# Optimization experiments

Measured on AMD Instinct MI355X. Metric: run time of the kernel, lower is better.

The kernel has to match this reference:

```python
import jax, jax.numpy as jnp
import numpy as np

NUM_HEADS = 16


def setup_inputs() -> dict:
    key = jax.random.key(0)
    ks = jax.random.split(key, 9)
    B, N, E = 2, 2048, 1024
    s = 1.0 / np.sqrt(E).astype(np.float32)
    inp = {"x": jax.random.normal(ks[0], (B, N, E), jnp.float32)}
    names = ["q", "k", "v", "o"]
    for i, n in enumerate(names):
        inp[f"W{n}"] = jax.random.normal(ks[1 + 2 * i], (E, E), jnp.float32) * s
        inp[f"b{n}"] = jax.random.normal(ks[2 + 2 * i], (E,), jnp.float32) * 0.01
    return inp


def _feature(x):
    # act_fun = '1+elu'
    return jax.nn.elu(x) + 1.0


def reference(x, Wq, bq, Wk, bk, Wv, bv, Wo, bo):
    B, N, E = x.shape
    H = NUM_HEADS
    d = E // H

    def proj(t, W, b):  # torch nn.Linear: t @ W^T + b
        return t @ W.T + b

    def split_heads(t):  # (B,N,E) -> (B,H,N,d)
        return t.reshape(B, N, H, d).transpose(0, 2, 1, 3)

    q = _feature(split_heads(proj(x, Wq, bq)))
    k = _feature(split_heads(proj(x, Wk, bk)))
    v = split_heads(proj(x, Wv, bv))

    # causal linear attention: o_t = q_t @ cumsum_{s<=t} (k_s v_s^T)
    kv = jnp.cumsum(k[..., :, None] * v[..., None, :], axis=2)  # (B,H,N,d,d)
    o = jnp.einsum('bhnd,bhnde->bhne', q, kv)                   # (B,H,N,d)

    o = o.transpose(0, 2, 1, 3).reshape(B, N, E)
    return o @ Wo.T + bo
```

## Files before the change

kernel.cpp:

```cpp
#include <hip/hip_runtime.h>
#include <hip/hip_bf16.h>
#include <cmath>

typedef unsigned short u16;
typedef __bf16 bf16x8 __attribute__((ext_vector_type(8)));
typedef float  f32x4  __attribute__((ext_vector_type(4)));
typedef float  f4     __attribute__((ext_vector_type(4)));
typedef u16    us4    __attribute__((ext_vector_type(4)));

#define DEVFN __device__ __forceinline__

static constexpr int Bq = 2, Nq = 2048, Eq = 1024;
static constexpr int Mq = Bq * Nq;
static constexpr int CHK = 64;
static constexpr int NC  = Nq / CHK;
static constexpr int BH  = Bq * 16;

DEVFN u16 f2b(float f) {
    union { float f; unsigned int u; } x; x.f = f;
    unsigned int r = x.u + 0x7fffu + ((x.u >> 16) & 1u);
    return (u16)(r >> 16);
}
DEVFN float b2f(u16 v) {
    union { unsigned int u; float f; } x; x.u = ((unsigned int)v) << 16; return x.f;
}

DEVFN void gl_lds16(const u16* g, u16* l) {
    __builtin_amdgcn_global_load_lds(
        (const __attribute__((address_space(1))) unsigned int*)(g),
        (__attribute__((address_space(3))) unsigned int*)(l),
        16, 0, 0);
}

__global__ __launch_bounds__(256)
void cvt_all_kernel(const float* __restrict__ x,
                    const float* __restrict__ w0, const float* __restrict__ w1,
                    const float* __restrict__ w2, const float* __restrict__ w3,
                    u16* __restrict__ Xb, u16* __restrict__ Wb)
{
    const int blk = blockIdx.x;
    const float* s; u16* d; int i;
    if (blk < 4096) {
        i = blk * 256 + threadIdx.x;  s = x;  d = Xb;
    } else {
        const int wsel = (blk - 4096) >> 10;
        i = ((blk - 4096) & 1023) * 256 + threadIdx.x;
        s = (wsel == 0) ? w0 : (wsel == 1) ? w1 : (wsel == 2) ? w2 : w3;
        d = Wb + (size_t)wsel * (Eq * Eq);
    }
    f4 v = *reinterpret_cast<const f4*>(&s[(size_t)i * 4]);
    us4 p; p[0] = f2b(v[0]); p[1] = f2b(v[1]); p[2] = f2b(v[2]); p[3] = f2b(v[3]);
    *reinterpret_cast<us4*>(&d[(size_t)i * 4]) = p;
}

__global__ __launch_bounds__(512, 4)
void qkv_ring(const u16* __restrict__ X, const u16* __restrict__ W,
              const float* __restrict__ b0, const float* __restrict__ b1,
              const float* __restrict__ b2,
              u16* __restrict__ Qb, u16* __restrict__ Kb, u16* __restrict__ KbT,
              u16* __restrict__ VbT)
{
    constexpr int BUFU = 16384;
    __shared__ u16 lds[2 * BUFU];
    const int tid = threadIdx.x, wid = tid >> 6, lane = tid & 63;
    const int wr = (wid >> 1) * 32, wc = (wid & 1) * 64;
    const int fr = lane & 15, fq = lane >> 4;

    const int bid = blockIdx.x;
    const int fid = (bid & 7) * 96 + (bid >> 3);
    const int bx = fid % 24, by = fid / 24;
    const int m0 = by * 128, n0 = bx * 128;

    const int row0 = tid >> 3;
    const int sc   = ((tid & 7) ^ (row0 & 7)) * 8;
    const u16* gA = X + (size_t)(m0 + row0) * 1024 + sc;
    const u16* gB = W + (size_t)(n0 + row0) * 1024 + sc;
    const int dw = wid * 512;

    int aoff[2][2], boff[2][4];
#pragma unroll
    for (int kk = 0; kk < 2; ++kk) {
        const int slot = ((kk * 4 + fq) ^ (fr & 7)) << 3;
#pragma unroll
        for (int mi = 0; mi < 2; ++mi)
            aoff[kk][mi] = (wr + mi * 16 + fr) * 64 + slot;
#pragma unroll
        for (int ni = 0; ni < 4; ++ni)
            boff[kk][ni] = 8192 + (wc + ni * 16 + fr) * 64 + slot;
    }

#define STAGE(kt, bs) do { u16* _b = lds + (bs) * BUFU;                        \
        gl_lds16(gA + (kt) * 64,              _b + dw);                        \
        gl_lds16(gA + (kt) * 64 + 64 * 1024,  _b + 4096 + dw);                 \
        gl_lds16(gB + (kt) * 64,              _b + 8192 + dw);                 \
        gl_lds16(gB + (kt) * 64 + 64 * 1024,  _b + 12288 + dw); } while (0)

    STAGE(0, 0);
    asm volatile("s_waitcnt vmcnt(0)" ::: "memory");
    __builtin_amdgcn_sched_barrier(0);
    __builtin_amdgcn_s_barrier();

    f32x4 acc[2][4] = {};

    for (int t = 0; t < 16; ++t) {
        if (t + 1 < 16) STAGE(t + 1, (t + 1) & 1);
        const u16* buf = lds + (t & 1) * BUFU;
#pragma unroll
        for (int kk = 0; kk < 2; ++kk) {
            bf16x8 af[2], bfv[4];
#pragma unroll
            for (int mi = 0; mi < 2; ++mi)
                af[mi] = *reinterpret_cast<const bf16x8*>(&buf[aoff[kk][mi]]);
#pragma unroll
            for (int ni = 0; ni < 4; ++ni)
                bfv[ni] = *reinterpret_cast<const bf16x8*>(&buf[boff[kk][ni]]);
            __builtin_amdgcn_s_setprio(1);
#pragma unroll
            for (int mi = 0; mi < 2; ++mi)
#pragma unroll
                for (int ni = 0; ni < 4; ++ni)
                    acc[mi][ni] = __builtin_amdgcn_mfma_f32_16x16x32_bf16(
                        af[mi], bfv[ni], acc[mi][ni], 0, 0, 0);
            __builtin_amdgcn_s_setprio(0);
        }
        asm volatile("s_waitcnt vmcnt(0)" ::: "memory");
        __builtin_amdgcn_sched_barrier(0);
        __builtin_amdgcn_s_barrier();
    }
#undef STAGE

    const int nw  = n0 + wc;
    const int seg = nw >> 10;
    const float* bp = (seg == 0) ? b0 : (seg == 1) ? b1 : b2;
#pragma unroll
    for (int mi = 0; mi < 2; ++mi)
#pragma unroll
        for (int ni = 0; ni < 4; ++ni) {
            const int nl    = (nw & 1023) + ni * 16 + fr;
            const int mbase = m0 + wr + mi * 16 + fq * 4;
            const float bn  = bp[nl];
            float vr[4];
#pragma unroll
            for (int r = 0; r < 4; ++r) {
                float v = acc[mi][ni][r] + bn;
                if (seg < 2) v = (v > 0.f) ? (v + 1.f) : __expf(v);
                vr[r] = v;
            }
            if (seg == 0) {
#pragma unroll
                for (int r = 0; r < 4; ++r)
                    Qb[(size_t)(mbase + r) * 1024 + nl] = f2b(vr[r]);
            } else {
                us4 pk;
#pragma unroll
                for (int r = 0; r < 4; ++r) pk[r] = f2b(vr[r]);
                const int bb = mbase >> 11, nt = mbase & 2047;
                const int hh = nl >> 6,     dd = nl & 63;
                u16* T = (seg == 1) ? KbT : VbT;
                *reinterpret_cast<us4*>(
                    &T[((size_t)(bb * 16 + hh) * 64 + dd) * 2048 + nt]) = pk;
                if (seg == 1) {
#pragma unroll
                    for (int r = 0; r < 4; ++r)
                        Kb[(size_t)(mbase + r) * 1024 + nl] = f2b(vr[r]);
                }
            }
        }
}

__global__ __launch_bounds__(256)
void oproj_kernel(const u16* __restrict__ X, const u16* __restrict__ W,
                  const float* __restrict__ b0, float* __restrict__ outF)
{
    constexpr int BUFU = (64 + 128) * 32;
    __shared__ u16 lds[3 * BUFU];
    const int tid = threadIdx.x, wid = tid >> 6, lane = tid & 63;
    const int wr = (wid >> 1) * 32, wc = (wid & 1) * 64;
    const int fr = lane & 15, fq = lane >> 4;

    const int bid = blockIdx.x;
    const int fid = (bid & 7) * 64 + (bid >> 3);
    const int bx = fid & 7, by = fid >> 3;
    const int m0 = by * 64, n0 = bx * 128;

    const int ra = tid >> 2;
    const int sc = ((tid & 3) ^ ((tid >> 3) & 3)) * 8;
    const u16* gA = X + (size_t)(m0 + ra) * 1024 + sc;
    const u16* gB = W + (size_t)(n0 + ra) * 1024 + sc;
    const int dw = wid * 512;

    const int fsw = (fq ^ ((fr >> 1) & 3)) << 3;
    int aoff[2], boff[4];
#pragma unroll
    for (int mi = 0; mi < 2; ++mi) aoff[mi] = (wr + mi * 16 + fr) * 32 + fsw;
#pragma unroll
    for (int ni = 0; ni < 4; ++ni) boff[ni] = 2048 + (wc + ni * 16 + fr) * 32 + fsw;

#define STAGE(kt, bs) do { u16* _b = lds + (bs) * BUFU;                          \
        gl_lds16(gA + (kt) * 32,             _b + dw);                           \
        gl_lds16(gB + (kt) * 32,             _b + 2048 + dw);                    \
        gl_lds16(gB + (kt) * 32 + 64 * 1024, _b + 4096 + dw); } while (0)

    STAGE(0, 0);
    STAGE(1, 1);
    asm volatile("s_waitcnt vmcnt(3)" ::: "memory");
    __builtin_amdgcn_sched_barrier(0);
    __builtin_amdgcn_s_barrier();

    f32x4 acc[2][4] = {};
    int cb = 0, sb = 2;

    for (int t = 0; t < 32; ++t) {
        if (t + 2 < 32) STAGE(t + 2, sb);
        const u16* buf = lds + cb * BUFU;
        bf16x8 af[2], bfv[4];
#pragma unroll
        for (int mi = 0; mi < 2; ++mi)
            af[mi] = *reinterpret_cast<const bf16x8*>(&buf[aoff[mi]]);
#pragma unroll
        for (int ni = 0; ni < 4; ++ni)
            bfv[ni] = *reinterpret_cast<const bf16x8*>(&buf[boff[ni]]);
        __builtin_amdgcn_s_setprio(1);
#pragma unroll
        for (int mi = 0; mi < 2; ++mi)
#pragma unroll
            for (int ni = 0; ni < 4; ++ni)
                acc[mi][ni] = __builtin_amdgcn_mfma_f32_16x16x32_bf16(
                    af[mi], bfv[ni], acc[mi][ni], 0, 0, 0);
        __builtin_amdgcn_s_setprio(0);
        if (t < 30)       asm volatile("s_waitcnt vmcnt(3)" ::: "memory");
        else if (t == 30) asm volatile("s_waitcnt vmcnt(0)" ::: "memory");
        __builtin_amdgcn_sched_barrier(0);
        __builtin_amdgcn_s_barrier();
        cb = (cb == 2) ? 0 : cb + 1;
        sb = (sb == 2) ? 0 : sb + 1;
    }
#undef STAGE

#pragma unroll
    for (int mi = 0; mi < 2; ++mi)
#pragma unroll
        for (int ni = 0; ni < 4; ++ni) {
            const int n     = n0 + wc + ni * 16 + fr;
            const int mbase = m0 + wr + mi * 16 + fq * 4;
            const float bn  = b0[n];
#pragma unroll
            for (int r = 0; r < 4; ++r)
                outF[(size_t)(mbase + r) * 1024 + n] = acc[mi][ni][r] + bn;
        }
}

__global__ __launch_bounds__(64)
void chunk_kv_kernel(const u16* __restrict__ KbT, const u16* __restrict__ VbT,
                     u16* __restrict__ KVT)
{
    const int blk = blockIdx.x;
    const int nh = blk & 1;
    const int bc = blk >> 1;
    const int bh = bc >> 5, c = bc & 31;
    const int lane = threadIdx.x;
    const int fr = lane & 15, fq = lane >> 4, fk = fq * 8;
    const u16* kt = KbT + (size_t)bh * 64 * 2048;
    const u16* vt = VbT + (size_t)bh * 64 * 2048;

    bf16x8 a[4][2], b[2][2];
#pragma unroll
    for (int mi = 0; mi < 4; ++mi)
#pragma unroll
        for (int kh = 0; kh < 2; ++kh)
            a[mi][kh] = *reinterpret_cast<const bf16x8*>(
                &vt[(size_t)(mi * 16 + fr) * 2048 + c * 64 + kh * 32 + fk]);
#pragma unroll
    for (int ni = 0; ni < 2; ++ni)
#pragma unroll
        for (int kh = 0; kh < 2; ++kh)
            b[ni][kh] = *reinterpret_cast<const bf16x8*>(
                &kt[(size_t)((nh * 2 + ni) * 16 + fr) * 2048 + c * 64 + kh * 32 + fk]);

    f32x4 acc[4][2] = {};
    __builtin_amdgcn_s_setprio(1);
#pragma unroll
    for (int mi = 0; mi < 4; ++mi)
#pragma unroll
        for (int ni = 0; ni < 2; ++ni)
#pragma unroll
            for (int kh = 0; kh < 2; ++kh)
                acc[mi][ni] = __builtin_amdgcn_mfma_f32_16x16x32_bf16(
                    a[mi][kh], b[ni][kh], acc[mi][ni], 0, 0, 0);
    __builtin_amdgcn_s_setprio(0);

    u16* out = KVT + (size_t)bc * 4096;
#pragma unroll
    for (int mi = 0; mi < 4; ++mi)
#pragma unroll
        for (int ni = 0; ni < 2; ++ni)
#pragma unroll
            for (int r = 0; r < 4; ++r)
                out[(mi * 16 + fq * 4 + r) * 64 + (nh * 2 + ni) * 16 + fr] =
                    f2b(acc[mi][ni][r]);
}

__global__ __launch_bounds__(256)
void scan_kernel(const u16* __restrict__ KVT, u16* __restrict__ STb)
{
    const int bh = blockIdx.x >> 4, sl = blockIdx.x & 15;
    const int el = sl * 256 + threadIdx.x;
    const u16* src = KVT + (size_t)bh * NC * 4096 + el;
    u16*      dst  = STb + (size_t)bh * NC * 4096 + el;
    float run = 0.f;
#pragma unroll 4
    for (int c = 0; c < NC; ++c) {
        dst[(size_t)c * 4096] = f2b(run);
        run += b2f(src[(size_t)c * 4096]);
    }
}

__global__ __launch_bounds__(128)
void attn_kernel(const u16* __restrict__ Qb, const u16* __restrict__ Kb,
                 const u16* __restrict__ VbT, const u16* __restrict__ STb,
                 u16* __restrict__ Ob)
{
    __shared__ u16 P[64 * 72];
    const int blk = blockIdx.x;
    const int bh = blk >> 5, c = blk & 31;
    const int b = bh >> 4, h = bh & 15;
    const int tid = threadIdx.x, wv = tid >> 6, lane = tid & 63;
    const int fr = lane & 15, fq = lane >> 4, fk = fq * 8;
    const int tok0 = b * 2048 + c * 64;

    bf16x8 qa[4][2];
#pragma unroll
    for (int mi = 0; mi < 4; ++mi)
#pragma unroll
        for (int kh = 0; kh < 2; ++kh)
            qa[mi][kh] = *reinterpret_cast<const bf16x8*>(
                &Qb[(size_t)(tok0 + mi * 16 + fr) * 1024 + h * 64 + kh * 32 + fk]);

    {
        bf16x8 kb[2][2];
#pragma unroll
        for (int si = 0; si < 2; ++si)
#pragma unroll
            for (int kh = 0; kh < 2; ++kh)
                kb[si][kh] = *reinterpret_cast<const bf16x8*>(
                    &Kb[(size_t)(tok0 + (wv * 2 + si) * 16 + fr) * 1024
                        + h * 64 + kh * 32 + fk]);
        f32x4 p[4][2] = {};
        __builtin_amdgcn_s_setprio(1);
#pragma unroll
        for (int mi = 0; mi < 4; ++mi)
#pragma unroll
            for (int si = 0; si < 2; ++si)
#pragma unroll
                for (int kh = 0; kh < 2; ++kh)
                    p[mi][si] = __builtin_amdgcn_mfma_f32_16x16x32_bf16(
                        qa[mi][kh], kb[si][kh], p[mi][si], 0, 0, 0);
        __builtin_amdgcn_s_setprio(0);
#pragma unroll
        for (int mi = 0; mi < 4; ++mi)
#pragma unroll
            for (int si = 0; si < 2; ++si)
#pragma unroll
                for (int r = 0; r < 4; ++r) {
                    int t = mi * 16 + fq * 4 + r;
                    int s = (wv * 2 + si) * 16 + fr;
                    float v = (s <= t) ? p[mi][si][r] : 0.0f;
                    P[t * 72 + s] = f2b(v);
                }
    }
    __syncthreads();

    f32x4 acc[4][2] = {};
    {
        const u16* st = STb + (size_t)blk * 4096;
        bf16x8 sb[2][2];
#pragma unroll
        for (int ni = 0; ni < 2; ++ni)
#pragma unroll
            for (int kh = 0; kh < 2; ++kh)
                sb[ni][kh] = *reinterpret_cast<const bf16x8*>(
                    &st[((wv * 2 + ni) * 16 + fr) * 64 + kh * 32 + fk]);
        __builtin_amdgcn_s_setprio(1);
#pragma unroll
        for (int mi = 0; mi < 4; ++mi)
#pragma unroll
            for (int ni = 0; ni < 2; ++ni)
#pragma unroll
                for (int kh = 0; kh < 2; ++kh)
                    acc[mi][ni] = __builtin_amdgcn_mfma_f32_16x16x32_bf16(
                        qa[mi][kh], sb[ni][kh], acc[mi][ni], 0, 0, 0);
        __builtin_amdgcn_s_setprio(0);
    }
    {
        const u16* vt = VbT + (size_t)bh * 64 * 2048;
#pragma unroll
        for (int sh = 0; sh < 2; ++sh) {
            bf16x8 pa[4], vb[2];
#pragma unroll
            for (int mi = 0; mi < 4; ++mi)
                pa[mi] = *reinterpret_cast<const bf16x8*>(
                    &P[(mi * 16 + fr) * 72 + sh * 32 + fk]);
#pragma unroll
            for (int ni = 0; ni < 2; ++ni)
                vb[ni] = *reinterpret_cast<const bf16x8*>(
                    &vt[(size_t)((wv * 2 + ni) * 16 + fr) * 2048
                        + c * 64 + sh * 32 + fk]);
            __builtin_amdgcn_s_setprio(1);
#pragma unroll
            for (int mi = 0; mi < 4; ++mi)
#pragma unroll
                for (int ni = 0; ni < 2; ++ni)
                    acc[mi][ni] = __builtin_amdgcn_mfma_f32_16x16x32_bf16(
                        pa[mi], vb[ni], acc[mi][ni], 0, 0, 0);
            __builtin_amdgcn_s_setprio(0);
        }
    }
#pragma unroll
    for (int mi = 0; mi < 4; ++mi)
#pragma unroll
        for (int ni = 0; ni < 2; ++ni)
#pragma unroll
            for (int r = 0; r < 4; ++r) {
                int t = tok0 + mi * 16 + fq * 4 + r;
                int n = h * 64 + (wv * 2 + ni) * 16 + fr;
                Ob[(size_t)t * 1024 + n] = f2b(acc[mi][ni][r]);
            }
}

extern "C" void kernel_launch(void* const* d_in, const int* in_sizes, int n_in,
                              void* d_out, int out_size, void* d_ws, size_t ws_size,
                              hipStream_t stream)
{
    (void)in_sizes; (void)n_in; (void)out_size; (void)ws_size;
    const float* x  = (const float*)d_in[0];
    const float* Wq = (const float*)d_in[1];
    const float* bq = (const float*)d_in[2];
    const float* Wk = (const float*)d_in[3];
    const float* bk = (const float*)d_in[4];
    const float* Wv = (const float*)d_in[5];
    const float* bv = (const float*)d_in[6];
    const float* Wo = (const float*)d_in[7];
    const float* bo = (const float*)d_in[8];
    float* out = (float*)d_out;

    char* ws = (char*)d_ws;
    constexpr size_t SZ_ME = (size_t)Mq * Eq * 2;
    u16*   Qb  = (u16*)  (ws + 0 * SZ_ME);
    u16*   Kb  = (u16*)  (ws + 1 * SZ_ME);
    u16*   KbT = (u16*)  (ws + 2 * SZ_ME);
    u16*   VbT = (u16*)  (ws + 3 * SZ_ME);
    u16*   Ob  = (u16*)  (ws + 4 * SZ_ME);
    u16*   KVT = (u16*)  (ws + 5 * SZ_ME);
    u16*   STb = (u16*)  (ws + 6 * SZ_ME);
    u16*   Xb  = (u16*)  (ws + 7 * SZ_ME);
    u16*   Wb0 = (u16*)  (ws + 8 * SZ_ME);
    u16* Wqkvb = Wb0;
    u16* Wob   = Wb0 + (size_t)3 * Eq * Eq;

    cvt_all_kernel<<<dim3(8192), dim3(256), 0, stream>>>(x, Wq, Wk, Wv, Wo, Xb, Wb0);

    qkv_ring<<<dim3(768), dim3(512), 0, stream>>>(
        Xb, Wqkvb, bq, bk, bv, Qb, Kb, KbT, VbT);

    chunk_kv_kernel<<<dim3(BH * NC * 2), dim3(64), 0, stream>>>(KbT, VbT, KVT);
    scan_kernel<<<dim3(BH * 16), dim3(256), 0, stream>>>(KVT, STb);
    attn_kernel<<<dim3(BH * NC), dim3(128), 0, stream>>>(Qb, Kb, VbT, STb, Ob);

    oproj_kernel<<<dim3(512), dim3(256), 0, stream>>>(Ob, Wob, bo, out);
}
```

Baseline: 89.28 us.

## Restructure output projection GEMM to 512 threads with BK=64 double buffering

The output projection kernel now runs 8 waves per block instead of 4. Each wave computes a 16x64 sub-tile, and the block tile stays 64x128. K-step depth doubles to 64 with a new XOR swizzle, and the triple-buffered pipeline becomes double buffering with a full vmcnt(0) wait every iteration. The aim is more waves in flight and half as many loop iterations and barriers, at the cost of less prefetch depth and less per-wave register reuse.

Result: faster. 86.79 us (-2.8%).

```diff
diff --git a/kernel.cpp b/kernel.cpp
--- a/kernel.cpp
+++ b/kernel.cpp
@@ -168,14 +168,14 @@
         }
 }
 
-__global__ __launch_bounds__(256)
+__global__ __launch_bounds__(512, 4)
 void oproj_kernel(const u16* __restrict__ X, const u16* __restrict__ W,
                   const float* __restrict__ b0, float* __restrict__ outF)
 {
-    constexpr int BUFU = (64 + 128) * 32;
-    __shared__ u16 lds[3 * BUFU];
+    constexpr int BUFU = 12288;
+    __shared__ u16 lds[2 * BUFU];
     const int tid = threadIdx.x, wid = tid >> 6, lane = tid & 63;
-    const int wr = (wid >> 1) * 32, wc = (wid & 1) * 64;
+    const int wr = (wid >> 1) * 16, wc = (wid & 1) * 64;
     const int fr = lane & 15, fq = lane >> 4;
 
     const int bid = blockIdx.x;
@@ -183,71 +183,66 @@
     const int bx = fid & 7, by = fid >> 3;
     const int m0 = by * 64, n0 = bx * 128;
 
-    const int ra = tid >> 2;
-    const int sc = ((tid & 3) ^ ((tid >> 3) & 3)) * 8;
-    const u16* gA = X + (size_t)(m0 + ra) * 1024 + sc;
-    const u16* gB = W + (size_t)(n0 + ra) * 1024 + sc;
+    const int row0 = tid >> 3;
+    const int sc   = ((tid & 7) ^ (row0 & 7)) * 8;
+    const u16* gA = X + (size_t)(m0 + row0) * 1024 + sc;
+    const u16* gB = W + (size_t)(n0 + row0) * 1024 + sc;
     const int dw = wid * 512;
 
-    const int fsw = (fq ^ ((fr >> 1) & 3)) << 3;
-    int aoff[2], boff[4];
-#pragma unroll
-    for (int mi = 0; mi < 2; ++mi) aoff[mi] = (wr + mi * 16 + fr) * 32 + fsw;
-#pragma unroll
-    for (int ni = 0; ni < 4; ++ni) boff[ni] = 2048 + (wc + ni * 16 + fr) * 32 + fsw;
-
-#define STAGE(kt, bs) do { u16* _b = lds + (bs) * BUFU;                          \
-        gl_lds16(gA + (kt) * 32,             _b + dw);                           \
-        gl_lds16(gB + (kt) * 32,             _b + 2048 + dw);                    \
-        gl_lds16(gB + (kt) * 32 + 64 * 1024, _b + 4096 + dw); } while (0)
+    int aoff[2], boff[2][4];
+#pragma unroll
+    for (int kk = 0; kk < 2; ++kk) {
+        const int slot = ((kk * 4 + fq) ^ (fr & 7)) << 3;
+        aoff[kk] = (wr + fr) * 64 + slot;
+#pragma unroll
+        for (int ni = 0; ni < 4; ++ni)
+            boff[kk][ni] = 4096 + (wc + ni * 16 + fr) * 64 + slot;
+    }
+
+#define STAGE(kt, bs) do { u16* _b = lds + (bs) * BUFU;                        \
+        gl_lds16(gA + (kt) * 64,              _b + dw);                        \
+        gl_lds16(gB + (kt) * 64,              _b + 4096 + dw);                 \
+        gl_lds16(gB + (kt) * 64 + 64 * 1024,  _b + 8192 + dw); } while (0)
 
     STAGE(0, 0);
-    STAGE(1, 1);
-    asm volatile("s_waitcnt vmcnt(3)" ::: "memory");
+    asm volatile("s_waitcnt vmcnt(0)" ::: "memory");
     __builtin_amdgcn_sched_barrier(0);
     __builtin_amdgcn_s_barrier();
 
-    f32x4 acc[2][4] = {};
-    int cb = 0, sb = 2;
-
-    for (int t = 0; t < 32; ++t) {
-        if (t + 2 < 32) STAGE(t + 2, sb);
-        const u16* buf = lds + cb * BUFU;
-        bf16x8 af[2], bfv[4];
-#pragma unroll
-        for (int mi = 0; mi < 2; ++mi)
-            af[mi] = *reinterpret_cast<const bf16x8*>(&buf[aoff[mi]]);
-#pragma unroll
-        for (int ni = 0; ni < 4; ++ni)
-            bfv[ni] = *reinterpret_cast<const bf16x8*>(&buf[boff[ni]]);
-        __builtin_amdgcn_s_setprio(1);
-#pragma unroll
-        for (int mi = 0; mi < 2; ++mi)
+    f32x4 acc[4] = {};
+
+    for (int t = 0; t < 16; ++t) {
+        if (t + 1 < 16) STAGE(t + 1, (t + 1) & 1);
+        const u16* buf = lds + (t & 1) * BUFU;
+#pragma unroll
+        for (int kk = 0; kk < 2; ++kk) {
+            bf16x8 af, bfv[4];
+            af = *reinterpret_cast<const bf16x8*>(&buf[aoff[kk]]);
 #pragma unroll
             for (int ni = 0; ni < 4; ++ni)
-                acc[mi][ni] = __builtin_amdgcn_mfma_f32_16x16x32_bf16(
-                    af[mi], bfv[ni], acc[mi][ni], 0, 0, 0);
-        __builtin_amdgcn_s_setprio(0);
-        if (t < 30)       asm volatile("s_waitcnt vmcnt(3)" ::: "memory");
-        else if (t == 30) asm volatile("s_waitcnt vmcnt(0)" ::: "memory");
+                bfv[ni] = *reinterpret_cast<const bf16x8*>(&buf[boff[kk][ni]]);
+            __builtin_amdgcn_s_setprio(1);
+#pragma unroll
+            for (int ni = 0; ni < 4; ++ni)
+                acc[ni] = __builtin_amdgcn_mfma_f32_16x16x32_bf16(
+                    af, bfv[ni], acc[ni], 0, 0, 0);
+            __builtin_amdgcn_s_setprio(0);
+        }
+        asm volatile("s_waitcnt vmcnt(0)" ::: "memory");
         __builtin_amdgcn_sched_barrier(0);
         __builtin_amdgcn_s_barrier();
-        cb = (cb == 2) ? 0 : cb + 1;
-        sb = (sb == 2) ? 0 : sb + 1;
     }
 #undef STAGE
 
 #pragma unroll
-    for (int mi = 0; mi < 2; ++mi)
-#pragma unroll
-        for (int ni = 0; ni < 4; ++ni) {
-            const int n     = n0 + wc + ni * 16 + fr;
-            const int mbase = m0 + wr + mi * 16 + fq * 4;
-            const float bn  = b0[n];
-#pragma unroll
-            for (int r = 0; r < 4; ++r)
-                outF[(size_t)(mbase + r) * 1024 + n] = acc[mi][ni][r] + bn;
-        }
+    for (int ni = 0; ni < 4; ++ni) {
+        const int n     = n0 + wc + ni * 16 + fr;
+        const int mbase = m0 + wr + fq * 4;
+        const float bn  = b0[n];
+#pragma unroll
+        for (int r = 0; r < 4; ++r)
+            outF[(size_t)(mbase + r) * 1024 + n] = acc[ni][r] + bn;
+    }
 }
 
 __global__ __launch_bounds__(64)
@@ -466,5 +461,5 @@
     scan_kernel<<<dim3(BH * 16), dim3(256), 0, stream>>>(KVT, STb);
     attn_kernel<<<dim3(BH * NC), dim3(128), 0, stream>>>(Qb, Kb, VbT, STb, Ob);
 
-    oproj_kernel<<<dim3(512), dim3(256), 0, stream>>>(Ob, Wob, bo, out);
-}
+    oproj_kernel<<<dim3(512), dim3(512), 0, stream>>>(Ob, Wob, bo, out);
+}
```
